# Kernel optimization log

Measured on AMD Instinct MI355X. Metric: run time of the kernel, lower is better.

## Reference

```python
import jax, jax.numpy as jnp
import numpy as np

B, S, E, H = 2, 2048, 512, 8
HD = E // H  # head dim = 64


def setup_inputs() -> dict:
    key = jax.random.key(0)
    k1, k2, k3 = jax.random.split(key, 3)
    scale_qkv = (6.0 / (E + 3 * E)) ** 0.5  # xavier-uniform-like scale
    scale_o = (6.0 / (E + E)) ** 0.5
    return {
        "X": jax.random.normal(k1, (B, S, E), dtype=jnp.float32),
        "Wqkv": jax.random.uniform(k2, (E, 3 * E), jnp.float32, -scale_qkv, scale_qkv),
        "bqkv": jnp.zeros((3 * E,), jnp.float32),
        "Wo": jax.random.uniform(k3, (E, E), jnp.float32, -scale_o, scale_o),
        "bo": jnp.zeros((E,), jnp.float32),
    }


def reference(X, Wqkv, bqkv, Wo, bo):
    b, s, e = X.shape
    # qkv projection: [B,S,3E] -> [B,S,H,3*HD] -> [B,H,S,3*HD]
    qkv = X @ Wqkv + bqkv
    qkv = qkv.reshape(b, s, H, 3 * HD).transpose(0, 2, 1, 3)
    q, k, v = jnp.array_split(qkv, 3, axis=-1)  # each [B,H,S,HD]
    # naive scaled dot-product attention (full score matrix, per source)
    attn_logits = jnp.einsum("bhqd,bhkd->bhqk", q, k) / jnp.sqrt(jnp.float32(HD))
    attention = jax.nn.softmax(attn_logits, axis=-1)  # [B,H,S,S]
    values = jnp.einsum("bhqk,bhkd->bhqd", attention, v)
    values = values.transpose(0, 2, 1, 3).reshape(b, s, e)
    o = values @ Wo + bo
    return (o, attention)
```

## Files before the change

kernel.cpp:

```cpp
#include <hip/hip_runtime.h>

typedef unsigned short u16;
typedef u16 u16x2 __attribute__((ext_vector_type(2)));
typedef u16 u16x4 __attribute__((ext_vector_type(4)));
typedef u16 u16x8 __attribute__((ext_vector_type(8)));
typedef __bf16 bf16x8 __attribute__((ext_vector_type(8)));
typedef float f32x4 __attribute__((ext_vector_type(4)));
typedef float f32x2 __attribute__((ext_vector_type(2)));

#define MFMA16(A, B, C) __builtin_amdgcn_mfma_f32_16x16x32_bf16(A, B, C, 0, 0, 0)

#define SB 2
#define SS 2048
#define SE 512
#define SH 8
#define SHD 64

__device__ __forceinline__ u16 f2b(float f) {
  return __builtin_bit_cast(u16, (__bf16)f);
}

__device__ __forceinline__ bf16x8 as_bf16x8(u16x8 v) {
  return __builtin_bit_cast(bf16x8, v);
}

__global__ __launch_bounds__(256)
void prep_kernel(const float* __restrict__ X, u16* __restrict__ Xb,
                 const float* __restrict__ Wqkv, u16* __restrict__ WqkvT)
{
  __shared__ float t[32][33];
  const int tid = threadIdx.x;
  if (blockIdx.x < 2048) {
    const int i = (blockIdx.x * 256 + tid) * 4;
    const float4 v = *(const float4*)&X[i];
    u16x4 o;
    o[0] = f2b(v.x); o[1] = f2b(v.y); o[2] = f2b(v.z); o[3] = f2b(v.w);
    *(u16x4*)&Xb[i] = o;
  } else {
    const int bx = blockIdx.x - 2048;
    const int n0 = (bx % 48) * 32, k0 = (bx / 48) * 32;
    const int r = tid >> 3, c4 = (tid & 7) * 4;
    const float4 v = *(const float4*)&Wqkv[(size_t)(k0 + r) * 1536 + n0 + c4];
    t[r][c4 + 0] = v.x; t[r][c4 + 1] = v.y; t[r][c4 + 2] = v.z; t[r][c4 + 3] = v.w;
    __syncthreads();
    u16x4 o;
    o[0] = f2b(t[c4 + 0][r]);
    o[1] = f2b(t[c4 + 1][r]);
    o[2] = f2b(t[c4 + 2][r]);
    o[3] = f2b(t[c4 + 3][r]);
    *(u16x4*)&WqkvT[(n0 + r) * 512 + k0 + c4] = o;
  }
}

__global__ __launch_bounds__(256)
void wtrans_kernel(const float* __restrict__ in, u16* __restrict__ out, int N)
{
  __shared__ float t[32][33];
  const int tid = threadIdx.x;
  const int r = tid >> 3, c4 = (tid & 7) * 4;
  const int k0 = blockIdx.y * 32, n0 = blockIdx.x * 32;
  const float4 v = *(const float4*)&in[(size_t)(k0 + r) * N + n0 + c4];
  t[r][c4 + 0] = v.x; t[r][c4 + 1] = v.y; t[r][c4 + 2] = v.z; t[r][c4 + 3] = v.w;
  __syncthreads();
  u16x4 o;
  o[0] = f2b(t[c4 + 0][r]);
  o[1] = f2b(t[c4 + 1][r]);
  o[2] = f2b(t[c4 + 2][r]);
  o[3] = f2b(t[c4 + 3][r]);
  *(u16x4*)&out[(n0 + r) * 512 + k0 + c4] = o;
}

template <int MODE>
__global__ __launch_bounds__(256, 2)
void gemm_kernel(const u16* __restrict__ A, const u16* __restrict__ Bt,
                 const float* __restrict__ bias,
                 u16* __restrict__ Q, u16* __restrict__ K, u16* __restrict__ Vt,
                 float* __restrict__ Out)
{
  __shared__ __align__(16) u16 As[128 * 40];
  __shared__ __align__(16) u16 Bs[128 * 40];
  const int tid  = threadIdx.x;
  const int lane = tid & 63, wave = tid >> 6, quad = lane >> 4, l16 = lane & 15;
  const int m0 = blockIdx.y * 128, n0 = blockIdx.x * 128;
  const int wr = (wave >> 1) * 64, wc = (wave & 1) * 64;
  const int sr = tid >> 2, sc = (tid & 3) * 8;

  const f32x4 z4 = {0.f, 0.f, 0.f, 0.f};
  f32x4 acc[4][4];
#pragma unroll
  for (int i = 0; i < 4; i++)
#pragma unroll
    for (int j = 0; j < 4; j++) acc[i][j] = z4;

  for (int k0 = 0; k0 < 512; k0 += 32) {
    const u16x8 a0 = *(const u16x8*)&A[(m0 + sr) * 512 + k0 + sc];
    const u16x8 a1 = *(const u16x8*)&A[(m0 + 64 + sr) * 512 + k0 + sc];
    const u16x8 b0 = *(const u16x8*)&Bt[(n0 + sr) * 512 + k0 + sc];
    const u16x8 b1 = *(const u16x8*)&Bt[(n0 + 64 + sr) * 512 + k0 + sc];
    __syncthreads();
    *(u16x8*)&As[sr * 40 + sc]        = a0;
    *(u16x8*)&As[(64 + sr) * 40 + sc] = a1;
    *(u16x8*)&Bs[sr * 40 + sc]        = b0;
    *(u16x8*)&Bs[(64 + sr) * 40 + sc] = b1;
    __syncthreads();
    bf16x8 af[4], bf[4];
#pragma unroll
    for (int i = 0; i < 4; i++) {
      af[i] = as_bf16x8(*(const u16x8*)&As[(wr + i * 16 + l16) * 40 + quad * 8]);
      bf[i] = as_bf16x8(*(const u16x8*)&Bs[(wc + i * 16 + l16) * 40 + quad * 8]);
    }
#pragma unroll
    for (int i = 0; i < 4; i++)
#pragma unroll
      for (int j = 0; j < 4; j++) acc[i][j] = MFMA16(af[i], bf[j], acc[i][j]);
  }

#pragma unroll
  for (int tm = 0; tm < 4; tm++) {
#pragma unroll
    for (int tn = 0; tn < 4; tn++) {
#pragma unroll
      for (int r = 0; r < 4; r++) {
        const int gm = m0 + wr + tm * 16 + quad * 4 + r;
        const int gn = n0 + wc + tn * 16 + l16;
        const float v = acc[tm][tn][r] + bias[gn];
        if (MODE == 0) {
          const int bb = gm >> 11, s = gm & 2047;
          const int hh = gn / 192, j = gn - hh * 192;
          const int bh = bb * SH + hh;
          if (j < 64)
            Q[(bh * SS + s) * SHD + j] = f2b(v * 0.125f);
          else if (j < 128)
            K[(bh * SS + s) * SHD + (j - 64)] = f2b(v);
          else
            Vt[(bh * SHD + (j - 128)) * SS + s] = f2b(v);
        } else {
          Out[gm * 512 + gn] = v;
        }
      }
    }
  }
}

#define PSTR 264
#define PWAVE (16 * PSTR)
#define OSTR 72

__global__ __launch_bounds__(512, 4)
void attn_kernel(const u16* __restrict__ Q, const u16* __restrict__ K,
                 const u16* __restrict__ Vt, u16* __restrict__ values,
                 float* __restrict__ attn)
{
  __shared__ __align__(16) u16 p_lds[8 * PWAVE];
  __shared__ float srm[8][16];
  __shared__ float srl[8][16];

  const int tid  = threadIdx.x;
  const int lane = tid & 63, wave = tid >> 6, quad = lane >> 4, l16 = lane & 15;

  const int bid = blockIdx.x;
  const int wg  = (bid & 7) * 256 + (bid >> 3);
  const int qt  = wg & 127;
  const int bh  = wg >> 7;
  const int h = bh & 7, b = bh >> 3;
  const int q0 = qt * 16;

  const u16* Qb = Q + (size_t)bh * SS * SHD;
  const u16* Kb = K + (size_t)bh * SS * SHD;
  const u16* Vb = Vt + (size_t)bh * SHD * SS;

  const bf16x8 aq0 = as_bf16x8(*(const u16x8*)&Qb[(q0 + l16) * SHD + quad * 8]);
  const bf16x8 aq1 = as_bf16x8(*(const u16x8*)&Qb[(q0 + l16) * SHD + 32 + quad * 8]);

  f32x4 acc[16];
#pragma unroll
  for (int ct = 0; ct < 16; ct++) {
    const int kb = wave * 256 + ct * 16;
    bf16x8 bk0 = as_bf16x8(*(const u16x8*)&Kb[(kb + l16) * SHD + quad * 8]);
    bf16x8 bk1 = as_bf16x8(*(const u16x8*)&Kb[(kb + l16) * SHD + 32 + quad * 8]);
    f32x4 c = {0.f, 0.f, 0.f, 0.f};
    c = MFMA16(bk0, aq0, c);
    c = MFMA16(bk1, aq1, c);
    acc[ct] = c;
  }

  f32x4 mx4 = acc[0];
#pragma unroll
  for (int ct = 1; ct < 16; ct++)
#pragma unroll
    for (int r = 0; r < 4; r++) mx4[r] = fmaxf(mx4[r], acc[ct][r]);
  float m = fmaxf(fmaxf(mx4[0], mx4[1]), fmaxf(mx4[2], mx4[3]));
  m = fmaxf(m, __shfl_xor(m, 16));
  m = fmaxf(m, __shfl_xor(m, 32));

  f32x4 s4 = {0.f, 0.f, 0.f, 0.f};
#pragma unroll
  for (int ct = 0; ct < 16; ct++)
#pragma unroll
    for (int r = 0; r < 4; r++) {
      const float p = __expf(acc[ct][r] - m);
      acc[ct][r] = p;
      s4[r] += p;
    }
  float s = (s4[0] + s4[1]) + (s4[2] + s4[3]);
  s += __shfl_xor(s, 16);
  s += __shfl_xor(s, 32);

  if (lane < 16) {
    srm[wave][l16] = m;
    srl[wave][l16] = s;
  }
  __syncthreads();

  float mg = srm[0][l16];
#pragma unroll
  for (int w = 1; w < 8; w++) mg = fmaxf(mg, srm[w][l16]);
  float lg = 0.f;
#pragma unroll
  for (int w = 0; w < 8; w++) lg += srl[w][l16] * __expf(srm[w][l16] - mg);
  const float scale = __expf(m - mg) / lg;
#pragma unroll
  for (int ct = 0; ct < 16; ct++)
#pragma unroll
    for (int r = 0; r < 4; r++) acc[ct][r] *= scale;

  u16* pl = &p_lds[wave * PWAVE];
#pragma unroll
  for (int ct = 0; ct < 16; ct++) {
    u16x4 t;
#pragma unroll
    for (int r = 0; r < 4; r++) t[r] = f2b(acc[ct][r]);
    *(u16x4*)&pl[l16 * PSTR + ct * 16 + quad * 4] = t;
  }

  f32x4 oacc[4];
#pragma unroll
  for (int nt = 0; nt < 4; nt++) oacc[nt] = (f32x4){0.f, 0.f, 0.f, 0.f};
  bf16x8 vbuf[2][4];
  {
    const int sb = wave * 256 + quad * 8;
#pragma unroll
    for (int nt = 0; nt < 4; nt++)
      vbuf[0][nt] = as_bf16x8(*(const u16x8*)&Vb[(nt * 16 + l16) * SS + sb]);
  }
#pragma unroll
  for (int kc = 0; kc < 8; kc++) {
    if (kc < 7) {
      const int sb = wave * 256 + (kc + 1) * 32 + quad * 8;
#pragma unroll
      for (int nt = 0; nt < 4; nt++)
        vbuf[(kc + 1) & 1][nt] =
            as_bf16x8(*(const u16x8*)&Vb[(nt * 16 + l16) * SS + sb]);
    }
    bf16x8 pa = as_bf16x8(*(const u16x8*)&pl[l16 * PSTR + kc * 32 + quad * 8]);
#pragma unroll
    for (int nt = 0; nt < 4; nt++)
      oacc[nt] = MFMA16(vbuf[kc & 1][nt], pa, oacc[nt]);
  }

  float* op = (float*)pl;
#pragma unroll
  for (int nt = 0; nt < 4; nt++)
    *(f32x4*)&op[l16 * OSTR + nt * 16 + quad * 4] = oacc[nt];
  __syncthreads();

  const int q = tid >> 5, d0 = (tid & 31) * 2;
  f32x2 s2 = {0.f, 0.f};
#pragma unroll
  for (int w = 0; w < 8; w++) {
    const float* opw = (const float*)&p_lds[w * PWAVE];
    s2 += *(const f32x2*)&opw[q * OSTR + d0];
  }
  u16x2 o2;
  o2[0] = f2b(s2[0]);
  o2[1] = f2b(s2[1]);
  *(u16x2*)&values[((size_t)(b * SS + q0 + q) * SH + h) * SHD + d0] = o2;

  float* attn_b = attn + ((size_t)bh * SS + q0) * SS;
#pragma unroll
  for (int ct = 0; ct < 16; ct++) {
    *(f32x4*)&attn_b[l16 * SS + wave * 256 + ct * 16 + quad * 4] = acc[ct];
  }
}

extern "C" void kernel_launch(void* const* d_in, const int* in_sizes, int n_in,
                              void* d_out, int out_size, void* d_ws, size_t ws_size,
                              hipStream_t stream) {
  const float* X    = (const float*)d_in[0];
  const float* Wqkv = (const float*)d_in[1];
  const float* bqkv = (const float*)d_in[2];
  const float* Wo   = (const float*)d_in[3];
  const float* bo   = (const float*)d_in[4];

  float* o_out    = (float*)d_out;
  float* attn_out = o_out + SB * SS * SE;

  const size_t QKV_ELEMS = (size_t)SB * SH * SS * SHD;
  u16* Q      = (u16*)d_ws;
  u16* K      = Q + QKV_ELEMS;
  u16* Vt     = K + QKV_ELEMS;
  u16* values = Vt + QKV_ELEMS;
  u16* Xb     = values;
  u16* WqkvT  = (u16*)attn_out;
  u16* WoT    = Q;

  prep_kernel<<<dim3(2816), 256, 0, stream>>>(X, Xb, Wqkv, WqkvT);

  gemm_kernel<0><<<dim3(12, 32), 256, 0, stream>>>(Xb, WqkvT, bqkv, Q, K, Vt, nullptr);
  attn_kernel<<<dim3(2048), 512, 0, stream>>>(Q, K, Vt, values, attn_out);
  wtrans_kernel<<<dim3(16, 16), 256, 0, stream>>>(Wo, WoT, 512);
  gemm_kernel<1><<<dim3(4, 32), 256, 0, stream>>>(values, WoT, bo,
                                                  nullptr, nullptr, nullptr, o_out);
}
```

Baseline: 423.4 us.

## Recompute QK scores in two passes to cut registers and raise occupancy

```diff
diff --git a/kernel.cpp b/kernel.cpp
--- a/kernel.cpp
+++ b/kernel.cpp
@@ -142,16 +142,16 @@
   }
 }
 
-#define PSTR 264
-#define PWAVE (16 * PSTR)
-#define OSTR 72
-
-__global__ __launch_bounds__(512, 4)
+#define PSTR2 136
+#define PWAVE2 (16 * PSTR2)
+#define OSTR2 68
+
+__global__ __launch_bounds__(512, 6)
 void attn_kernel(const u16* __restrict__ Q, const u16* __restrict__ K,
                  const u16* __restrict__ Vt, u16* __restrict__ values,
                  float* __restrict__ attn)
 {
-  __shared__ __align__(16) u16 p_lds[8 * PWAVE];
+  __shared__ __align__(16) u16 p_lds[8 * PWAVE2];
   __shared__ float srm[8][16];
   __shared__ float srl[8][16];
 
@@ -172,8 +172,7 @@
   const bf16x8 aq0 = as_bf16x8(*(const u16x8*)&Qb[(q0 + l16) * SHD + quad * 8]);
   const bf16x8 aq1 = as_bf16x8(*(const u16x8*)&Qb[(q0 + l16) * SHD + 32 + quad * 8]);
 
-  f32x4 acc[16];
-#pragma unroll
+  float m = -1e30f, l = 0.f;
   for (int ct = 0; ct < 16; ct++) {
     const int kb = wave * 256 + ct * 16;
     bf16x8 bk0 = as_bf16x8(*(const u16x8*)&Kb[(kb + l16) * SHD + quad * 8]);
@@ -181,34 +180,24 @@
     f32x4 c = {0.f, 0.f, 0.f, 0.f};
     c = MFMA16(bk0, aq0, c);
     c = MFMA16(bk1, aq1, c);
-    acc[ct] = c;
-  }
-
-  f32x4 mx4 = acc[0];
-#pragma unroll
-  for (int ct = 1; ct < 16; ct++)
-#pragma unroll
-    for (int r = 0; r < 4; r++) mx4[r] = fmaxf(mx4[r], acc[ct][r]);
-  float m = fmaxf(fmaxf(mx4[0], mx4[1]), fmaxf(mx4[2], mx4[3]));
-  m = fmaxf(m, __shfl_xor(m, 16));
-  m = fmaxf(m, __shfl_xor(m, 32));
-
-  f32x4 s4 = {0.f, 0.f, 0.f, 0.f};
-#pragma unroll
-  for (int ct = 0; ct < 16; ct++)
-#pragma unroll
-    for (int r = 0; r < 4; r++) {
-      const float p = __expf(acc[ct][r] - m);
-      acc[ct][r] = p;
-      s4[r] += p;
-    }
-  float s = (s4[0] + s4[1]) + (s4[2] + s4[3]);
-  s += __shfl_xor(s, 16);
-  s += __shfl_xor(s, 32);
-
+    const float tm = fmaxf(fmaxf(c[0], c[1]), fmaxf(c[2], c[3]));
+    const float mn = fmaxf(m, tm);
+    const float s = (__expf(c[0] - mn) + __expf(c[1] - mn)) +
+                    (__expf(c[2] - mn) + __expf(c[3] - mn));
+    l = l * __expf(m - mn) + s;
+    m = mn;
+  }
+#pragma unroll
+  for (int off = 16; off <= 32; off <<= 1) {
+    const float m2 = __shfl_xor(m, off);
+    const float l2 = __shfl_xor(l, off);
+    const float mn = fmaxf(m, m2);
+    l = l * __expf(m - mn) + l2 * __expf(m2 - mn);
+    m = mn;
+  }
   if (lane < 16) {
     srm[wave][l16] = m;
-    srl[wave][l16] = s;
+    srl[wave][l16] = l;
   }
   __syncthreads();
 
@@ -218,69 +207,64 @@
   float lg = 0.f;
 #pragma unroll
   for (int w = 0; w < 8; w++) lg += srl[w][l16] * __expf(srm[w][l16] - mg);
-  const float scale = __expf(m - mg) / lg;
-#pragma unroll
-  for (int ct = 0; ct < 16; ct++)
-#pragma unroll
-    for (int r = 0; r < 4; r++) acc[ct][r] *= scale;
-
-  u16* pl = &p_lds[wave * PWAVE];
-#pragma unroll
-  for (int ct = 0; ct < 16; ct++) {
-    u16x4 t;
-#pragma unroll
-    for (int r = 0; r < 4; r++) t[r] = f2b(acc[ct][r]);
-    *(u16x4*)&pl[l16 * PSTR + ct * 16 + quad * 4] = t;
-  }
-
+  const float inv = 1.f / lg;
+
+  u16* pl = &p_lds[wave * PWAVE2];
+  float* attn_b = attn + ((size_t)bh * SS + q0) * SS;
   f32x4 oacc[4];
 #pragma unroll
   for (int nt = 0; nt < 4; nt++) oacc[nt] = (f32x4){0.f, 0.f, 0.f, 0.f};
-  bf16x8 vbuf[2][4];
-  {
-    const int sb = wave * 256 + quad * 8;
-#pragma unroll
-    for (int nt = 0; nt < 4; nt++)
-      vbuf[0][nt] = as_bf16x8(*(const u16x8*)&Vb[(nt * 16 + l16) * SS + sb]);
-  }
-#pragma unroll
-  for (int kc = 0; kc < 8; kc++) {
-    if (kc < 7) {
-      const int sb = wave * 256 + (kc + 1) * 32 + quad * 8;
-#pragma unroll
-      for (int nt = 0; nt < 4; nt++)
-        vbuf[(kc + 1) & 1][nt] =
-            as_bf16x8(*(const u16x8*)&Vb[(nt * 16 + l16) * SS + sb]);
-    }
-    bf16x8 pa = as_bf16x8(*(const u16x8*)&pl[l16 * PSTR + kc * 32 + quad * 8]);
-#pragma unroll
-    for (int nt = 0; nt < 4; nt++)
-      oacc[nt] = MFMA16(vbuf[kc & 1][nt], pa, oacc[nt]);
+
+#pragma unroll
+  for (int half = 0; half < 2; half++) {
+#pragma unroll
+    for (int ct8 = 0; ct8 < 8; ct8++) {
+      const int ct = half * 8 + ct8;
+      const int kb = wave * 256 + ct * 16;
+      bf16x8 bk0 = as_bf16x8(*(const u16x8*)&Kb[(kb + l16) * SHD + quad * 8]);
+      bf16x8 bk1 = as_bf16x8(*(const u16x8*)&Kb[(kb + l16) * SHD + 32 + quad * 8]);
+      f32x4 c = {0.f, 0.f, 0.f, 0.f};
+      c = MFMA16(bk0, aq0, c);
+      c = MFMA16(bk1, aq1, c);
+      f32x4 p;
+      u16x4 t;
+#pragma unroll
+      for (int r = 0; r < 4; r++) {
+        p[r] = __expf(c[r] - mg) * inv;
+        t[r] = f2b(p[r]);
+      }
+      *(f32x4*)&attn_b[l16 * SS + ct * 16 + wave * 256 + quad * 4] = p;
+      *(u16x4*)&pl[l16 * PSTR2 + ct8 * 16 + quad * 4] = t;
+    }
+#pragma unroll
+    for (int kc = 0; kc < 4; kc++) {
+      bf16x8 pa = as_bf16x8(*(const u16x8*)&pl[l16 * PSTR2 + kc * 32 + quad * 8]);
+      const int sb = wave * 256 + half * 128 + kc * 32 + quad * 8;
+#pragma unroll
+      for (int nt = 0; nt < 4; nt++) {
+        bf16x8 vb = as_bf16x8(*(const u16x8*)&Vb[(nt * 16 + l16) * SS + sb]);
+        oacc[nt] = MFMA16(vb, pa, oacc[nt]);
+      }
+    }
   }
 
   float* op = (float*)pl;
 #pragma unroll
   for (int nt = 0; nt < 4; nt++)
-    *(f32x4*)&op[l16 * OSTR + nt * 16 + quad * 4] = oacc[nt];
+    *(f32x4*)&op[l16 * OSTR2 + nt * 16 + quad * 4] = oacc[nt];
   __syncthreads();
 
   const int q = tid >> 5, d0 = (tid & 31) * 2;
   f32x2 s2 = {0.f, 0.f};
 #pragma unroll
   for (int w = 0; w < 8; w++) {
-    const float* opw = (const float*)&p_lds[w * PWAVE];
-    s2 += *(const f32x2*)&opw[q * OSTR + d0];
+    const float* opw = (const float*)&p_lds[w * PWAVE2];
+    s2 += *(const f32x2*)&opw[q * OSTR2 + d0];
   }
   u16x2 o2;
   o2[0] = f2b(s2[0]);
   o2[1] = f2b(s2[1]);
   *(u16x2*)&values[((size_t)(b * SS + q0 + q) * SH + h) * SHD + d0] = o2;
-
-  float* attn_b = attn + ((size_t)bh * SS + q0) * SS;
-#pragma unroll
-  for (int ct = 0; ct < 16; ct++) {
-    *(f32x4*)&attn_b[l16 * SS + wave * 256 + ct * 16 + quad * 4] = acc[ct];
-  }
 }
 
 extern "C" void kernel_launch(void* const* d_in, const int* in_sizes, int n_in,
```

After: 467.5 us. +10.4%, slower.
